# Kernel optimization log

Measured on AMD Instinct MI355X. Metric: run time of the kernel, lower is better.

Reference implementation:

```python
import jax, jax.numpy as jnp
from jax import lax
import numpy as np

N = 256          # HiPPO order
DT = 1.0 / 4096  # discretization step ~ 1/L
L = 4096         # sequence length
BATCH = 64


def _legt_transition(n):
    # LegT (translated Legendre) HiPPO transition matrices (continuous-time).
    Q = np.arange(n, dtype=np.float64)
    R = (2.0 * Q + 1.0) ** 0.5
    j, i = np.meshgrid(Q, Q)
    A = R[:, None] * np.where(i < j, (-1.0) ** (i - j), 1.0) * R[None, :]
    B = R[:, None]
    return -A, B


def _bilinear_discretize(A, B, dt):
    # scipy.signal.cont2discrete(..., method='bilinear')
    n = A.shape[0]
    I = np.eye(n)
    M = np.linalg.inv(I - (dt / 2.0) * A)
    Ad = M @ (I + (dt / 2.0) * A)
    Bd = (M @ B) * dt
    return Ad, Bd


def setup_inputs() -> dict:
    key = jax.random.key(0)
    A, B = _legt_transition(N)
    Ad, Bd = _bilinear_discretize(A, B, DT)
    inputs = jax.random.normal(key, (L, BATCH), dtype=jnp.float32)
    return {
        "inputs": inputs,
        "A": jnp.asarray(Ad, dtype=jnp.float32),          # (N, N)
        "B": jnp.asarray(Bd.squeeze(-1), dtype=jnp.float32),  # (N,)
    }


def reference(inputs, A, B):
    # inputs: (L, BATCH) -> output cs: (L, BATCH, N)
    u = inputs[..., None]  # (L, BATCH, 1)
    c0 = jnp.zeros((inputs.shape[1], A.shape[0]), dtype=inputs.dtype)  # (BATCH, N)

    def step(c, f):
        # c = F.linear(c, A) + B * f  ==  c @ A^T + B * f
        c = c @ A.T + B * f
        return c, c

    _, cs = lax.scan(step, c0, u)
    return cs
```

## Files before the change

### kernel.cpp

```cpp
#include <hip/hip_runtime.h>
#include <hip/hip_bf16.h>


#define MATF 65536

typedef __attribute__((ext_vector_type(8))) short short8;
typedef __attribute__((ext_vector_type(4))) float f32x4;

__device__ __forceinline__ unsigned short f2bf(float x) {
  union { __hip_bfloat16 h; unsigned short u; } cv;
  cv.h = __float2bfloat16(x);
  return cv.u;
}
__device__ __forceinline__ float bf2f(unsigned short u) {
  union { unsigned short u; __hip_bfloat16 h; } cv;
  cv.u = u;
  return __bfloat162float(cv.h);
}

__device__ __forceinline__ void load16_lds(const void* gsrc, void* ldst) {
  __builtin_amdgcn_global_load_lds(
      (const __attribute__((address_space(1))) unsigned int*)gsrc,
      (__attribute__((address_space(3))) unsigned int*)ldst,
      16, 0, 0);
}

__global__ __launch_bounds__(256) void gemm_nn_batch(
    const float* __restrict__ X, const float* __restrict__ Ys,
    float* __restrict__ Zs, int count)
{
  int g    = blockIdx.x >> 4;
  int tile = blockIdx.x & 15;
  if (g >= count) return;
  const float* Y = Ys + (size_t)g * MATF;
  float*       Z = Zs + (size_t)g * MATF;
  int tr = (tile >> 2) * 64;
  int tc = (tile & 3) * 64;

  __shared__ float As[64][33];
  __shared__ float Bs[32][65];
  int tid = threadIdx.x;
  int tx = tid & 15, ty = tid >> 4;
  float acc[4][4] = {};

  for (int k0 = 0; k0 < 256; k0 += 32) {
#pragma unroll
    for (int p = 0; p < 2; ++p) {
      int idx = tid + p * 256;
      int r = idx >> 3, c4 = (idx & 7) * 4;
      float4 v = *(const float4*)(X + (size_t)(tr + r) * 256 + k0 + c4);
      As[r][c4 + 0] = v.x; As[r][c4 + 1] = v.y; As[r][c4 + 2] = v.z; As[r][c4 + 3] = v.w;
    }
#pragma unroll
    for (int p = 0; p < 2; ++p) {
      int idx = tid + p * 256;
      int r = idx >> 4, c4 = (idx & 15) * 4;
      float4 v = *(const float4*)(Y + (size_t)(k0 + r) * 256 + tc + c4);
      Bs[r][c4 + 0] = v.x; Bs[r][c4 + 1] = v.y; Bs[r][c4 + 2] = v.z; Bs[r][c4 + 3] = v.w;
    }
    __syncthreads();
#pragma unroll
    for (int kk = 0; kk < 32; ++kk) {
      float a[4], b[4];
#pragma unroll
      for (int u = 0; u < 4; ++u) a[u] = As[ty * 4 + u][kk];
#pragma unroll
      for (int v = 0; v < 4; ++v) b[v] = Bs[kk][tx * 4 + v];
#pragma unroll
      for (int u = 0; u < 4; ++u)
#pragma unroll
        for (int v = 0; v < 4; ++v) acc[u][v] += a[u] * b[v];
    }
    __syncthreads();
  }
#pragma unroll
  for (int u = 0; u < 4; ++u)
#pragma unroll
    for (int v = 0; v < 4; ++v)
      Z[(size_t)(tr + ty * 4 + u) * 256 + tc + tx * 4 + v] = acc[u][v];
}

__global__ __launch_bounds__(256) void kv_kernel(
    const float* __restrict__ P, const float* __restrict__ Bv,
    float* __restrict__ Kv)
{
  int j = blockIdx.x;
  int n = threadIdx.x;
  __shared__ float bs[256];
  bs[n] = Bv[n];
  __syncthreads();
  if (j == 0) { Kv[n] = bs[n]; return; }
  const float* M = P + (size_t)(j - 1) * MATF;
  float acc = 0.f;
  for (int m = 0; m < 256; ++m) acc += M[(size_t)n * 256 + m] * bs[m];
  Kv[(size_t)j * 256 + n] = acc;
}

__global__ __launch_bounds__(256) void e_kernel(
    const float* __restrict__ in, const float* __restrict__ Kv,
    float* __restrict__ e)
{
  int k = blockIdx.x >> 6;
  int b = blockIdx.x & 63;
  int n = threadIdx.x;
  __shared__ float fs[64];
  if (n < 64) fs[n] = in[(size_t)(k * 64 + n) * 64 + b];
  __syncthreads();
  float acc = 0.f;
#pragma unroll
  for (int j = 0; j < 64; ++j) acc += Kv[(size_t)j * 256 + n] * fs[63 - j];
  e[((size_t)k * 256 + n) * 64 + b] = acc;
}

__global__ __launch_bounds__(256) void scan_round(
    const float* __restrict__ win, float* __restrict__ wout,
    const float* __restrict__ M, int d,
    float* __restrict__ MSdst,
    const float* __restrict__ P, const float* __restrict__ Kv,
    unsigned short* __restrict__ Gt, int gt_row0, int gt_off)
{
  __shared__ float As[64][33];
  __shared__ float Bs[32][65];
  int bid = blockIdx.x;
  int tid = threadIdx.x;

  if (bid >= gt_off) {
    int r2 = gt_row0 + (bid - gt_off);
    if (r2 >= 16384) return;
    int i = r2 >> 8, n = r2 & 255;
    unsigned short* dst = Gt + (size_t)r2 * 640;
    for (int c = tid; c < 320; c += 256) {
      float x;
      if (c < 64) x = (c <= i) ? Kv[(size_t)(i - c) * 256 + n] : 0.f;
      else        x = P[(size_t)i * MATF + (size_t)n * 256 + (c - 64)];
      unsigned short hi = f2bf(x);
      float lo = x - bf2f(hi);
      dst[c]       = hi;
      dst[320 + c] = f2bf(lo);
    }
    return;
  }
  if (bid >= 256) {
    int tile = bid - 256;
    int tr = (tile >> 2) * 64;
    int tc = (tile & 3) * 64;
    int tx = tid & 15, ty = tid >> 4;
    float acc[4][4] = {};
    for (int k0 = 0; k0 < 256; k0 += 32) {
#pragma unroll
      for (int p = 0; p < 2; ++p) {
        int idx = tid + p * 256;
        int r = idx >> 3, c4 = (idx & 7) * 4;
        float4 v = *(const float4*)(M + (size_t)(tr + r) * 256 + k0 + c4);
        As[r][c4 + 0] = v.x; As[r][c4 + 1] = v.y; As[r][c4 + 2] = v.z; As[r][c4 + 3] = v.w;
      }
#pragma unroll
      for (int p = 0; p < 2; ++p) {
        int idx = tid + p * 256;
        int r = idx >> 4, c4 = (idx & 15) * 4;
        float4 v = *(const float4*)(M + (size_t)(k0 + r) * 256 + tc + c4);
        Bs[r][c4 + 0] = v.x; Bs[r][c4 + 1] = v.y; Bs[r][c4 + 2] = v.z; Bs[r][c4 + 3] = v.w;
      }
      __syncthreads();
#pragma unroll
      for (int kk = 0; kk < 32; ++kk) {
        float a[4], b[4];
#pragma unroll
        for (int u = 0; u < 4; ++u) a[u] = As[ty * 4 + u][kk];
#pragma unroll
        for (int v = 0; v < 4; ++v) b[v] = Bs[kk][tx * 4 + v];
#pragma unroll
        for (int u = 0; u < 4; ++u)
#pragma unroll
          for (int v = 0; v < 4; ++v) acc[u][v] += a[u] * b[v];
      }
      __syncthreads();
    }
#pragma unroll
    for (int u = 0; u < 4; ++u)
#pragma unroll
      for (int v = 0; v < 4; ++v)
        MSdst[(size_t)(tr + ty * 4 + u) * 256 + tc + tx * 4 + v] = acc[u][v];
    return;
  }

  int k  = bid >> 2;
  int rt = bid & 3;
  const float* src = win  + (size_t)k * 16384;
  float*       dst = wout + (size_t)k * 16384;
  if (k < d) {
#pragma unroll
    for (int p = 0; p < 16; ++p) {
      int idx = rt * 4096 + p * 256 + tid;
      dst[idx] = src[idx];
    }
    return;
  }
  const float* v = win + (size_t)(k - d) * 16384;
  int tx = tid & 15, ty = tid >> 4;
  float acc[4][4] = {};
  for (int k0 = 0; k0 < 256; k0 += 32) {
#pragma unroll
    for (int p = 0; p < 2; ++p) {
      int idx = tid + p * 256;
      int r = idx >> 3, c4 = (idx & 7) * 4;
      float4 t4 = *(const float4*)(M + (size_t)(rt * 64 + r) * 256 + k0 + c4);
      As[r][c4 + 0] = t4.x; As[r][c4 + 1] = t4.y; As[r][c4 + 2] = t4.z; As[r][c4 + 3] = t4.w;
    }
#pragma unroll
    for (int p = 0; p < 2; ++p) {
      int idx = tid + p * 256;
      int r = idx >> 4, c4 = (idx & 15) * 4;
      float4 t4 = *(const float4*)(v + (size_t)(k0 + r) * 64 + c4);
      Bs[r][c4 + 0] = t4.x; Bs[r][c4 + 1] = t4.y; Bs[r][c4 + 2] = t4.z; Bs[r][c4 + 3] = t4.w;
    }
    __syncthreads();
#pragma unroll
    for (int kk = 0; kk < 32; ++kk) {
      float a[4], b[4];
#pragma unroll
      for (int u = 0; u < 4; ++u) a[u] = As[ty * 4 + u][kk];
#pragma unroll
      for (int v2 = 0; v2 < 4; ++v2) b[v2] = Bs[kk][tx * 4 + v2];
#pragma unroll
      for (int u = 0; u < 4; ++u)
#pragma unroll
        for (int v2 = 0; v2 < 4; ++v2) acc[u][v2] += a[u] * b[v2];
    }
    __syncthreads();
  }
#pragma unroll
  for (int u = 0; u < 4; ++u)
#pragma unroll
    for (int v2 = 0; v2 < 4; ++v2) {
      int idx = (rt * 64 + ty * 4 + u) * 64 + tx * 4 + v2;
      dst[idx] = src[idx] + acc[u][v2];
    }
}

__global__ __launch_bounds__(320) void build_ht(
    const float* __restrict__ in, const float* __restrict__ w,
    unsigned short* __restrict__ Ht)
{
  int row = blockIdx.x;
  int k = row >> 6, b = row & 63;
  int j = threadIdx.x;
  float x;
  if (j < 64) x = in[(size_t)(k * 64 + j) * 64 + b];
  else        x = (k > 0) ? w[((size_t)(k - 1) * 256 + (j - 64)) * 64 + b] : 0.f;
  unsigned short hi = f2bf(x);
  float lo = x - bf2f(hi);
  Ht[(size_t)row * 640 + j]       = hi;
  Ht[(size_t)row * 640 + 320 + j] = f2bf(lo);
}

__global__ __launch_bounds__(256) void out_gemm(
    const unsigned short* __restrict__ Ht,
    const unsigned short* __restrict__ Gt,
    float* __restrict__ out)
{
  __shared__ unsigned short Asm[128 * 64];
  __shared__ unsigned short Bsm[128 * 64];

  int bid = blockIdx.x;
  int swz = (bid & 7) * 512 + (bid >> 3);
  int nt = swz >> 5;
  int mt = swz & 31;
  int mrow0 = mt * 128, nrow0 = nt * 128;

  int tid = threadIdx.x;
  int w = tid >> 6, l = tid & 63;
  int wm = w >> 1, wn = w & 1;

  char* Ab = (char*)Asm;
  char* Bb = (char*)Bsm;

  auto stage = [&](const unsigned short* src, int row0, char* lds, int k0) {
#pragma unroll
    for (int it = 0; it < 4; ++it) {
      int L = it * 4096 + tid * 16;
      int row = L >> 7;
      int p = (L >> 4) & 7;
      int o = p ^ (row & 7);
      int h = o >> 2, q = o & 3;
      const void* g = src + (size_t)(row0 + row) * 640 + h * 320 + k0 + q * 8;
      void* dst = lds + (it * 4096 + w * 1024);
      load16_lds(g, dst);
    }
  };

  stage(Ht, mrow0, Ab, 0);
  stage(Gt, nrow0, Bb, 0);

  f32x4 acc[4][4] = {};
  int rAbase = wm * 64 + (l & 15);
  int rBbase = wn * 64 + (l & 15);
  int qo = l >> 4;

  for (int ks = 0; ks < 10; ++ks) {
    __syncthreads();
    short8 ah[4], al[4], bh[4], bl[4];
#pragma unroll
    for (int mf = 0; mf < 4; ++mf) {
      int r = rAbase + mf * 16;
      int ph = (qo)     ^ (r & 7);
      int pl = (4 + qo) ^ (r & 7);
      ah[mf] = *(const short8*)(Ab + r * 128 + ph * 16);
      al[mf] = *(const short8*)(Ab + r * 128 + pl * 16);
    }
#pragma unroll
    for (int nf = 0; nf < 4; ++nf) {
      int r = rBbase + nf * 16;
      int ph = (qo)     ^ (r & 7);
      int pl = (4 + qo) ^ (r & 7);
      bh[nf] = *(const short8*)(Bb + r * 128 + ph * 16);
      bl[nf] = *(const short8*)(Bb + r * 128 + pl * 16);
    }
    __syncthreads();
    if (ks < 9) {
      stage(Ht, mrow0, Ab, (ks + 1) * 32);
      stage(Gt, nrow0, Bb, (ks + 1) * 32);
    }
#pragma unroll
    for (int mf = 0; mf < 4; ++mf)
#pragma unroll
      for (int nf = 0; nf < 4; ++nf) {
        acc[mf][nf] = __builtin_amdgcn_mfma_f32_16x16x32_bf16(ah[mf], bh[nf], acc[mf][nf], 0, 0, 0);
        acc[mf][nf] = __builtin_amdgcn_mfma_f32_16x16x32_bf16(ah[mf], bl[nf], acc[mf][nf], 0, 0, 0);
        acc[mf][nf] = __builtin_amdgcn_mfma_f32_16x16x32_bf16(al[mf], bh[nf], acc[mf][nf], 0, 0, 0);
      }
  }

  int Mbase = mrow0 + wm * 64 + (l >> 4) * 4;
  int Nbase = nrow0 + wn * 64 + (l & 15);
#pragma unroll
  for (int mf = 0; mf < 4; ++mf)
#pragma unroll
    for (int nf = 0; nf < 4; ++nf)
#pragma unroll
      for (int r = 0; r < 4; ++r) {
        int Mrow = Mbase + mf * 16 + r;
        int Ncol = Nbase + nf * 16;
        int k = Mrow >> 6, b = Mrow & 63;
        int i = Ncol >> 8, n = Ncol & 255;
        out[((size_t)k * 4096 + (size_t)i * 64 + b) * 256 + n] = acc[mf][nf][r];
      }
}

extern "C" void kernel_launch(void* const* d_in, const int* in_sizes, int n_in,
                              void* d_out, int out_size, void* d_ws, size_t ws_size,
                              hipStream_t stream)
{
  const float* in = (const float*)d_in[0];
  const float* A  = (const float*)d_in[1];
  const float* Bv = (const float*)d_in[2];
  float* out = (float*)d_out;
  float* ws  = (float*)d_ws;

  float* P  = ws;
  float* Kv = P  + (size_t)64 * MATF;
  float* e  = Kv + (size_t)64 * 256;
  float* w2 = e  + (size_t)64 * 16384;
  float* MS = w2 + (size_t)64 * 16384;
  unsigned short* Ht = (unsigned short*)(MS + (size_t)2 * MATF);
  unsigned short* Gt = Ht + (size_t)4096 * 640;

  hipMemcpyAsync(P, A, (size_t)MATF * sizeof(float),
                 hipMemcpyDeviceToDevice, stream);
  for (int m = 1; m <= 32; m <<= 1) {
    gemm_nn_batch<<<dim3(m * 16), dim3(256), 0, stream>>>(
        P + (size_t)(m - 1) * MATF, P, P + (size_t)m * MATF, m);
  }
  kv_kernel<<<dim3(64), dim3(256), 0, stream>>>(P, Bv, Kv);
  e_kernel<<<dim3(4096), dim3(256), 0, stream>>>(in, Kv, e);

  float* bufs[2] = {e, w2};
  for (int r = 0; r < 6; ++r) {
    const float* M = (r == 0) ? (P + (size_t)63 * MATF)
                              : (MS + (size_t)((r - 1) & 1) * MATF);
    float* MSdst = MS + (size_t)(r & 1) * MATF;
    int gt_row0 = r * 2731;
    int gt_cnt  = (r < 5) ? 2731 : (16384 - 5 * 2731);
    int gt_off  = (r < 5) ? 272 : 256;
    int grid    = gt_off + gt_cnt;
    scan_round<<<dim3(grid), dim3(256), 0, stream>>>(
        bufs[r & 1], bufs[(r + 1) & 1], M, 1 << r,
        MSdst, P, Kv, Gt, gt_row0, gt_off);
  }

  build_ht<<<dim3(4096), dim3(320), 0, stream>>>(in, e, Ht);

  out_gemm<<<dim3(4096), dim3(256), 0, stream>>>(Ht, Gt, out);
}
```

Baseline: 412.0 us.

## Double-buffer out_gemm LDS staging and fuse A copy with first power GEMM

out_gemm now keeps two LDS buffers and issues the global-to-LDS loads for the next K slice before reading the current one. This replaces the two barriers per iteration with one and lets the loads overlap the MFMA work. Separately, the device-to-device memcpy of A and the first squaring GEMM are merged into one pow_first kernel, which removes a copy command and a launch. The cost is twice the LDS (64KB per block), which may reduce occupancy. The new prefetch also relies on the trailing barrier to keep the next stage from overwriting a buffer that other waves are still reading.

```diff
diff --git a/kernel.cpp b/kernel.cpp
--- a/kernel.cpp
+++ b/kernel.cpp
@@ -78,6 +78,63 @@
 #pragma unroll
     for (int v = 0; v < 4; ++v)
       Z[(size_t)(tr + ty * 4 + u) * 256 + tc + tx * 4 + v] = acc[u][v];
+}
+
+__global__ __launch_bounds__(256) void pow_first(
+    const float* __restrict__ A, float* __restrict__ P)
+{
+  int bid = blockIdx.x, tid = threadIdx.x;
+  if (bid >= 16) {
+    int blk = bid - 16;
+#pragma unroll
+    for (int q = 0; q < 4; ++q) {
+      int idx = blk * 1024 + q * 256 + tid;
+      *(float4*)(P + (size_t)idx * 4) = *(const float4*)(A + (size_t)idx * 4);
+    }
+    return;
+  }
+  int tile = bid;
+  int tr = (tile >> 2) * 64;
+  int tc = (tile & 3) * 64;
+  __shared__ float As[64][33];
+  __shared__ float Bs[32][65];
+  int tx = tid & 15, ty = tid >> 4;
+  float acc[4][4] = {};
+  for (int k0 = 0; k0 < 256; k0 += 32) {
+#pragma unroll
+    for (int p = 0; p < 2; ++p) {
+      int idx = tid + p * 256;
+      int r = idx >> 3, c4 = (idx & 7) * 4;
+      float4 v = *(const float4*)(A + (size_t)(tr + r) * 256 + k0 + c4);
+      As[r][c4 + 0] = v.x; As[r][c4 + 1] = v.y; As[r][c4 + 2] = v.z; As[r][c4 + 3] = v.w;
+    }
+#pragma unroll
+    for (int p = 0; p < 2; ++p) {
+      int idx = tid + p * 256;
+      int r = idx >> 4, c4 = (idx & 15) * 4;
+      float4 v = *(const float4*)(A + (size_t)(k0 + r) * 256 + tc + c4);
+      Bs[r][c4 + 0] = v.x; Bs[r][c4 + 1] = v.y; Bs[r][c4 + 2] = v.z; Bs[r][c4 + 3] = v.w;
+    }
+    __syncthreads();
+#pragma unroll
+    for (int kk = 0; kk < 32; ++kk) {
+      float a[4], b[4];
+#pragma unroll
+      for (int u = 0; u < 4; ++u) a[u] = As[ty * 4 + u][kk];
+#pragma unroll
+      for (int v = 0; v < 4; ++v) b[v] = Bs[kk][tx * 4 + v];
+#pragma unroll
+      for (int u = 0; u < 4; ++u)
+#pragma unroll
+        for (int v = 0; v < 4; ++v) acc[u][v] += a[u] * b[v];
+    }
+    __syncthreads();
+  }
+#pragma unroll
+  for (int u = 0; u < 4; ++u)
+#pragma unroll
+    for (int v = 0; v < 4; ++v)
+      P[(size_t)MATF + (size_t)(tr + ty * 4 + u) * 256 + tc + tx * 4 + v] = acc[u][v];
 }
 
 __global__ __launch_bounds__(256) void kv_kernel(
@@ -259,8 +316,7 @@
     const unsigned short* __restrict__ Gt,
     float* __restrict__ out)
 {
-  __shared__ unsigned short Asm[128 * 64];
-  __shared__ unsigned short Bsm[128 * 64];
+  __shared__ char smem[65536];
 
   int bid = blockIdx.x;
   int swz = (bid & 7) * 512 + (bid >> 3);
@@ -271,9 +327,6 @@
   int tid = threadIdx.x;
   int w = tid >> 6, l = tid & 63;
   int wm = w >> 1, wn = w & 1;
-
-  char* Ab = (char*)Asm;
-  char* Bb = (char*)Bsm;
 
   auto stage = [&](const unsigned short* src, int row0, char* lds, int k0) {
 #pragma unroll
@@ -289,8 +342,9 @@
     }
   };
 
-  stage(Ht, mrow0, Ab, 0);
-  stage(Gt, nrow0, Bb, 0);
+  stage(Ht, mrow0, smem, 0);
+  stage(Gt, nrow0, smem + 16384, 0);
+  __syncthreads();
 
   f32x4 acc[4][4] = {};
   int rAbase = wm * 64 + (l & 15);
@@ -298,7 +352,14 @@
   int qo = l >> 4;
 
   for (int ks = 0; ks < 10; ++ks) {
-    __syncthreads();
+    char* cur = smem + (ks & 1) * 32768;
+    if (ks < 9) {
+      char* nxt = smem + ((ks + 1) & 1) * 32768;
+      stage(Ht, mrow0, nxt, (ks + 1) * 32);
+      stage(Gt, nrow0, nxt + 16384, (ks + 1) * 32);
+    }
+    char* Ab = cur;
+    char* Bb = cur + 16384;
     short8 ah[4], al[4], bh[4], bl[4];
 #pragma unroll
     for (int mf = 0; mf < 4; ++mf) {
@@ -316,11 +377,6 @@
       bh[nf] = *(const short8*)(Bb + r * 128 + ph * 16);
       bl[nf] = *(const short8*)(Bb + r * 128 + pl * 16);
     }
-    __syncthreads();
-    if (ks < 9) {
-      stage(Ht, mrow0, Ab, (ks + 1) * 32);
-      stage(Gt, nrow0, Bb, (ks + 1) * 32);
-    }
 #pragma unroll
     for (int mf = 0; mf < 4; ++mf)
 #pragma unroll
@@ -329,6 +385,7 @@
         acc[mf][nf] = __builtin_amdgcn_mfma_f32_16x16x32_bf16(ah[mf], bl[nf], acc[mf][nf], 0, 0, 0);
         acc[mf][nf] = __builtin_amdgcn_mfma_f32_16x16x32_bf16(al[mf], bh[nf], acc[mf][nf], 0, 0, 0);
       }
+    __syncthreads();
   }
 
   int Mbase = mrow0 + wm * 64 + (l >> 4) * 4;
@@ -365,9 +422,8 @@
   unsigned short* Ht = (unsigned short*)(MS + (size_t)2 * MATF);
   unsigned short* Gt = Ht + (size_t)4096 * 640;
 
-  hipMemcpyAsync(P, A, (size_t)MATF * sizeof(float),
-                 hipMemcpyDeviceToDevice, stream);
-  for (int m = 1; m <= 32; m <<= 1) {
+  pow_first<<<dim3(32), dim3(256), 0, stream>>>(A, P);
+  for (int m = 2; m <= 32; m <<= 1) {
     gemm_nn_batch<<<dim3(m * 16), dim3(256), 0, stream>>>(
         P + (size_t)(m - 1) * MATF, P, P + (size_t)m * MATF, m);
   }
```

Measured after the change: 404.8 us. Within noise of the previous version (-1.7%).
